# Performance work log

Hardware: AMD Instinct MI355X
Metric: run time of the kernel (lower is better)

## Reference

```python
import jax, jax.numpy as jnp
import numpy as np

B_SZ, L_SEQ, D_MODEL, D_STATE = 4, 2048, 1024, 16


def setup_inputs() -> dict:
    key = jax.random.key(0)
    ks = jax.random.split(key, 6)
    x = jax.random.normal(ks[0], (B_SZ, L_SEQ, D_MODEL), jnp.float32)
    # HiPPO-inspired init: A_log = log(arange(1..n)).clamp(min=-7), broadcast over channels
    A_log = jnp.clip(jnp.log(jnp.arange(1, D_STATE + 1, dtype=jnp.float32)), -7.0, None)
    A_log = jnp.broadcast_to(A_log[None, :], (D_MODEL, D_STATE)).astype(jnp.float32)
    B_param = 0.02 * jax.random.normal(ks[1], (D_MODEL, D_STATE), jnp.float32)
    C_param = 0.02 * jax.random.normal(ks[2], (D_MODEL, D_STATE), jnp.float32)
    log_dt = 0.01 * jax.random.normal(ks[3], (D_MODEL,), jnp.float32) - 4.0
    in_w = jax.random.normal(ks[4], (2 * D_MODEL, D_MODEL), jnp.float32) / np.sqrt(D_MODEL).astype(np.float32)
    in_b = jnp.zeros((2 * D_MODEL,), jnp.float32)
    out_w = jax.random.normal(ks[5], (D_MODEL, D_MODEL), jnp.float32) / np.sqrt(D_MODEL).astype(np.float32)
    out_b = jnp.zeros((D_MODEL,), jnp.float32)
    ln_g = jnp.ones((D_MODEL,), jnp.float32)
    ln_b = jnp.zeros((D_MODEL,), jnp.float32)
    return {"x": x, "A_log": A_log, "B_param": B_param, "C_param": C_param,
            "log_dt": log_dt, "in_w": in_w, "in_b": in_b, "out_w": out_w,
            "out_b": out_b, "ln_g": ln_g, "ln_b": ln_b}


def _ssm_scan(u, A_log, B_param, C_param, log_dt):
    # u: (B, L, D). Builds kernel h[t,d] = sum_n A_bar[d,n]^t * C[d,n]*B[d,n]*dt[d]
    # and applies a causal depthwise convolution (via FFT; same math as conv1d).
    L = u.shape[1]
    dt = jnp.clip(jnp.exp(log_dt), 1e-4, 1.0)                      # (D,)
    A_bar = jnp.exp(-jnp.exp(A_log) * dt[:, None])                 # ZOH discretisation (D,N)
    A_bar = jnp.clip(A_bar, 1e-8, 1.0 - 1e-8)
    log_A = jnp.log(A_bar)                                         # (D,N)
    t_idx = jnp.arange(L, dtype=jnp.float32)                       # (L,)
    A_powers = jnp.exp(t_idx[:, None, None] * log_A[None, :, :])   # (L,D,N)
    cb_dt = C_param * B_param * dt[:, None]                        # (D,N)
    kernel = jnp.einsum('ldn,dn->ld', A_powers, cb_dt)             # (L,D)
    # causal conv: y[b,t,d] = sum_{tau<=t} kernel[tau,d] * u[b,t-tau,d]
    n_fft = 2 * L
    Kf = jnp.fft.rfft(kernel, n=n_fft, axis=0)                     # (n_fft/2+1, D)
    Uf = jnp.fft.rfft(u, n=n_fft, axis=1)                          # (B, n_fft/2+1, D)
    y = jnp.fft.irfft(Uf * Kf[None], n=n_fft, axis=1)[:, :L]       # (B,L,D)
    return y.astype(u.dtype)


def reference(x, A_log, B_param, C_param, log_dt, in_w, in_b, out_w, out_b, ln_g, ln_b):
    x = x.astype(jnp.float32)
    residual = x
    # LayerNorm (eps=1e-5)
    mu = jnp.mean(x, axis=-1, keepdims=True)
    var = jnp.mean(jnp.square(x - mu), axis=-1, keepdims=True)
    xn = (x - mu) * jax.lax.rsqrt(var + 1e-5) * ln_g + ln_b
    xz = xn @ in_w.T + in_b                                        # (B,L,2D)
    x_proj, z = xz[..., :D_MODEL], xz[..., D_MODEL:]
    z = jax.nn.silu(z)
    y = _ssm_scan(x_proj, A_log, B_param, C_param, log_dt)
    y = y * z
    y = y @ out_w.T + out_b
    # dropout is identity in eval mode
    return jnp.clip(y + residual, -10.0, 10.0)
```

## Files before the change

kernel.cpp:

```cpp
#include <hip/hip_runtime.h>
#include <hip/hip_bf16.h>

#define D_MODEL 1024
#define D_STATE 16
#define L_SEQ 2048
#define B_SZ 4
#define M_ROWS (B_SZ * L_SEQ)
#define N_CHUNK 32
#define C_LEN 64

typedef __attribute__((ext_vector_type(8))) short short8;
typedef __attribute__((ext_vector_type(4))) float f32x4;

#define SBAR()  asm volatile("s_barrier" ::: "memory")
#define GATE(N) asm volatile("s_waitcnt vmcnt(" #N ") lgkmcnt(0)\n\ts_barrier" ::: "memory")

typedef const unsigned short __attribute__((address_space(1))) gas_us;
typedef unsigned short __attribute__((address_space(3))) las_us;
static __device__ __forceinline__ void gload16(const unsigned short* g, unsigned short* l) {
    __builtin_amdgcn_global_load_lds((gas_us*)g, (las_us*)l, 16, 0, 0);
}

static __device__ __forceinline__ unsigned short f2bf(float f) {
    unsigned int u = __float_as_uint(f);
    unsigned int r = (u + 0x7FFFu + ((u >> 16) & 1u)) >> 16;
    return (unsigned short)r;
}
static __device__ __forceinline__ float bf2f(unsigned short u) {
    return __uint_as_float(((unsigned int)u) << 16);
}

__global__ __launch_bounds__(256) void prep_kernel(const float* __restrict__ x,
                                                   const float* __restrict__ g,
                                                   const float* __restrict__ b,
                                                   unsigned short* __restrict__ xn,
                                                   const float* __restrict__ in_w,
                                                   unsigned short* __restrict__ w1,
                                                   const float* __restrict__ out_w,
                                                   unsigned short* __restrict__ w2) {
    __shared__ float sbuf[8];
    int bid = blockIdx.x;
    int t = threadIdx.x;
    if (bid < M_ROWS) {
        int row = bid;
        const float4* xr = (const float4*)(x + (size_t)row * D_MODEL);
        float4 v = xr[t];
        float s  = v.x + v.y + v.z + v.w;
        float ss = v.x * v.x + v.y * v.y + v.z * v.z + v.w * v.w;
        #pragma unroll
        for (int o = 32; o > 0; o >>= 1) {
            s  += __shfl_down(s,  o);
            ss += __shfl_down(ss, o);
        }
        int wid = t >> 6;
        if ((t & 63) == 0) { sbuf[wid] = s; sbuf[4 + wid] = ss; }
        __syncthreads();
        float S  = sbuf[0] + sbuf[1] + sbuf[2] + sbuf[3];
        float SS = sbuf[4] + sbuf[5] + sbuf[6] + sbuf[7];
        float mu  = S * (1.0f / D_MODEL);
        float var = SS * (1.0f / D_MODEL) - mu * mu;
        float inv = rsqrtf(var + 1e-5f);
        float4 gv = ((const float4*)g)[t];
        float4 bv = ((const float4*)b)[t];
        ushort4 o;
        o.x = f2bf((v.x - mu) * inv * gv.x + bv.x);
        o.y = f2bf((v.y - mu) * inv * gv.y + bv.y);
        o.z = f2bf((v.z - mu) * inv * gv.z + bv.z);
        o.w = f2bf((v.w - mu) * inv * gv.w + bv.w);
        ((ushort4*)(xn + (size_t)row * D_MODEL))[t] = o;
    } else if (bid < M_ROWS + 2048) {
        int i = (bid - M_ROWS) * 256 + t;
        float4 v = ((const float4*)in_w)[i];
        ushort4 o;
        o.x = f2bf(v.x); o.y = f2bf(v.y); o.z = f2bf(v.z); o.w = f2bf(v.w);
        ((ushort4*)w1)[i] = o;
    } else {
        int i = (bid - M_ROWS - 2048) * 256 + t;
        float4 v = ((const float4*)out_w)[i];
        ushort4 o;
        o.x = f2bf(v.x); o.y = f2bf(v.y); o.z = f2bf(v.z); o.w = f2bf(v.w);
        ((ushort4*)w2)[i] = o;
    }
}

#define MFMA32(ACC, AV, BV) { \
    _Pragma("unroll") for (int i_ = 0; i_ < 8; ++i_) { \
        _Pragma("unroll") for (int jf_ = 0; jf_ < 4; ++jf_) \
            ACC[i_][jf_] = __builtin_amdgcn_mfma_f32_16x16x32_bf16( \
                AV[i_], BV[jf_], ACC[i_][jf_], 0, 0, 0); } }

#define STAGE1(J) { size_t ko_ = (size_t)(J) * 32; int so_ = ((J) & 3) * 16384; \
    gload16(pA0 + ko_, dA0 + so_); gload16(pA1 + ko_, dA1 + so_); \
    gload16(pB0 + ko_, dB0 + so_); gload16(pB1 + ko_, dB1 + so_); }

#define G1_TILE(J, DOSTAGE, TRAIL) { \
    const int slot_ = (J) & 3; \
    const char* rA_ = ldsA_rd + slot_ * 32768; \
    const char* rB_ = ldsB_rd + slot_ * 32768; \
    short8 av[8], bv[4]; \
    _Pragma("unroll") for (int i_ = 0; i_ < 8; ++i_) av[i_] = *(const short8*)(rA_ + i_ * 1024); \
    _Pragma("unroll") for (int j_ = 0; j_ < 4; ++j_) bv[j_] = *(const short8*)(rB_ + j_ * 1024); \
    if (DOSTAGE) { STAGE1((J) + 3); } \
    SBAR(); \
    __builtin_amdgcn_s_setprio(1); \
    MFMA32(acc, av, bv); \
    __builtin_amdgcn_s_setprio(0); \
    TRAIL; \
}

__global__ __launch_bounds__(512, 1) void gemm1_kernel(const unsigned short* __restrict__ A,
                                                       const unsigned short* __restrict__ Bt,
                                                       const float* __restrict__ bias,
                                                       unsigned short* __restrict__ u_bf,
                                                       unsigned short* __restrict__ zs) {
    __shared__ __align__(16) unsigned short lds[4][16384];
    const int K = D_MODEL;

    int t = threadIdx.x;
    int lane = t & 63;
    int wave = t >> 6;
    int wm = wave >> 2;
    int wn = wave & 3;

    int bid = blockIdx.x;
    int swz = (bid & 7) * 32 + (bid >> 3);
    int m0 = (swz >> 3) * 256;
    int n0 = (swz & 7) * 256;

    int srow = lane >> 2;
    int sk = ((lane & 3) * 8) ^ ((lane & 32) >> 1);
    const unsigned short* pA0 = A  + (size_t)(m0 + wave * 16 + srow) * K + sk;
    const unsigned short* pA1 = pA0 + (size_t)128 * K;
    const unsigned short* pB0 = Bt + (size_t)(n0 + wave * 16 + srow) * K + sk;
    const unsigned short* pB1 = pB0 + (size_t)128 * K;

    unsigned short* dA0 = &lds[0][wave * 512];
    unsigned short* dA1 = &lds[0][4096 + wave * 512];
    unsigned short* dB0 = &lds[0][8192 + wave * 512];
    unsigned short* dB1 = &lds[0][12288 + wave * 512];

    int off_base = (lane & 15) * 64 + (((lane >> 4) * 16) ^ ((lane & 8) * 4));
    const char* ldsA_rd = (const char*)(&lds[0][0]) + wm * 8192 + off_base;
    const char* ldsB_rd = (const char*)(&lds[0][0]) + 16384 + wn * 4096 + off_base;

    f32x4 acc[8][4] = {};

    STAGE1(0); STAGE1(1); STAGE1(2);
    GATE(8);

    #pragma unroll 1
    for (int j = 0; j < 29; ++j) { G1_TILE(j, true, GATE(8)); }
    G1_TILE(29, false, GATE(4));
    G1_TILE(30, false, GATE(0));
    G1_TILE(31, false, (void)0);

    int col = lane & 15;
    int quad = lane >> 4;
    float bs[4];
    #pragma unroll
    for (int jf = 0; jf < 4; ++jf) bs[jf] = bias[n0 + wn * 64 + jf * 16 + col];
    bool isU = (n0 < D_MODEL);
    int nbase = isU ? (n0 + wn * 64 + col) : (n0 - D_MODEL + wn * 64 + col);
    unsigned short* obase = isU ? u_bf : zs;
    #pragma unroll
    for (int i = 0; i < 8; ++i) {
        #pragma unroll
        for (int r = 0; r < 4; ++r) {
            int m = m0 + wm * 128 + i * 16 + quad * 4 + r;
            unsigned short* orow = obase + (size_t)m * D_MODEL + nbase;
            #pragma unroll
            for (int jf = 0; jf < 4; ++jf) {
                float v = acc[i][jf][r] + bs[jf];
                if (!isU) v = v / (1.0f + __expf(-v));
                orow[jf * 16] = f2bf(v);
            }
        }
    }
}

#define MFMA16(ACC, AV, BV) { \
    _Pragma("unroll") for (int i_ = 0; i_ < 4; ++i_) { \
        _Pragma("unroll") for (int jf_ = 0; jf_ < 4; ++jf_) \
            ACC[i_][jf_] = __builtin_amdgcn_mfma_f32_16x16x32_bf16( \
                AV[i_], BV[jf_], ACC[i_][jf_], 0, 0, 0); } }

#define STAGE2(J) { size_t ko_ = (size_t)(J) * 32; int so_ = ((J) & 3) * 12288; \
    gload16(pA0 + ko_, dA + so_); gload16(pB0 + ko_, dB0 + so_); gload16(pB1 + ko_, dB1 + so_); }

#define G2_TILE(J, DOSTAGE, TRAIL) { \
    const int slot_ = (J) & 3; \
    const char* rA_ = ldsA_rd + slot_ * 24576; \
    const char* rB_ = ldsB_rd + slot_ * 24576; \
    short8 av[4], bv[4]; \
    _Pragma("unroll") for (int i_ = 0; i_ < 4; ++i_) av[i_] = *(const short8*)(rA_ + i_ * 1024); \
    _Pragma("unroll") for (int j_ = 0; j_ < 4; ++j_) bv[j_] = *(const short8*)(rB_ + j_ * 1024); \
    if (DOSTAGE) { STAGE2((J) + 3); } \
    SBAR(); \
    __builtin_amdgcn_s_setprio(1); \
    MFMA16(acc, av, bv); \
    __builtin_amdgcn_s_setprio(0); \
    TRAIL; \
}

__global__ __launch_bounds__(512, 2) void gemm2_kernel(const unsigned short* __restrict__ A,
                                                       const unsigned short* __restrict__ Bt,
                                                       const float* __restrict__ bias,
                                                       float* __restrict__ out_f,
                                                       const float* __restrict__ resid) {
    __shared__ __align__(16) unsigned short lds[4][12288];
    const int K = D_MODEL;

    int t = threadIdx.x;
    int lane = t & 63;
    int wave = t >> 6;
    int wm = wave >> 2;
    int wn = wave & 3;

    int bid = blockIdx.x;
    int swz = (bid & 7) * 32 + (bid >> 3);
    int m0 = (swz >> 2) * 128;
    int n0 = (swz & 3) * 256;

    int srow = lane >> 2;
    int sk = ((lane & 3) * 8) ^ ((lane & 32) >> 1);
    const unsigned short* pA0 = A  + (size_t)(m0 + wave * 16 + srow) * K + sk;
    const unsigned short* pB0 = Bt + (size_t)(n0 + wave * 16 + srow) * K + sk;
    const unsigned short* pB1 = pB0 + (size_t)128 * K;

    unsigned short* dA  = &lds[0][wave * 512];
    unsigned short* dB0 = &lds[0][4096 + wave * 512];
    unsigned short* dB1 = &lds[0][8192 + wave * 512];

    int off_base = (lane & 15) * 64 + (((lane >> 4) * 16) ^ ((lane & 8) * 4));
    const char* ldsA_rd = (const char*)(&lds[0][0]) + wm * 4096 + off_base;
    const char* ldsB_rd = (const char*)(&lds[0][0]) + 8192 + wn * 4096 + off_base;

    f32x4 acc[4][4] = {};

    STAGE2(0); STAGE2(1); STAGE2(2);
    GATE(6);

    #pragma unroll 1
    for (int j = 0; j < 29; ++j) { G2_TILE(j, true, GATE(6)); }
    G2_TILE(29, false, GATE(3));
    G2_TILE(30, false, GATE(0));
    G2_TILE(31, false, (void)0);

    int col = lane & 15;
    int quad = lane >> 4;
    float bs[4];
    #pragma unroll
    for (int jf = 0; jf < 4; ++jf) bs[jf] = bias[n0 + wn * 64 + jf * 16 + col];
    #pragma unroll
    for (int i = 0; i < 4; ++i) {
        #pragma unroll
        for (int r = 0; r < 4; ++r) {
            int m = m0 + wm * 64 + i * 16 + quad * 4 + r;
            const float* rrow = resid + (size_t)m * D_MODEL + n0 + wn * 64 + col;
            float* orow = out_f + (size_t)m * D_MODEL + n0 + wn * 64 + col;
            #pragma unroll
            for (int jf = 0; jf < 4; ++jf) {
                float y = acc[i][jf][r] + bs[jf] + rrow[jf * 16];
                y = fminf(10.0f, fmaxf(-10.0f, y));
                orow[jf * 16] = y;
            }
        }
    }
}

__global__ __launch_bounds__(512) void scan_fused_kernel(const unsigned short* __restrict__ u,
                                                         const unsigned short* __restrict__ zs,
                                                         const float* __restrict__ A_log,
                                                         const float* __restrict__ Bp,
                                                         const float* __restrict__ Cp,
                                                         const float* __restrict__ log_dt,
                                                         unsigned short* __restrict__ yz) {
    __shared__ float S[N_CHUNK][D_STATE][17];

    int bid = blockIdx.x;
    int l  = (bid & 7) * 32 + (bid >> 3);
    int b  = l >> 6;
    int dg = l & 63;
    int t  = threadIdx.x;
    int c  = t >> 4;
    int dl = t & 15;
    int d  = dg * 16 + dl;

    float dt = fminf(1.0f, fmaxf(1e-4f, __expf(log_dt[d])));
    float ab[D_STATE];
    #pragma unroll
    for (int n = 0; n < D_STATE; n++) {
        float a = __expf(-__expf(A_log[d * D_STATE + n]) * dt);
        ab[n] = fminf(1.0f - 1e-8f, fmaxf(1e-8f, a));
    }

    size_t row0 = (size_t)(b * L_SEQ + c * C_LEN);
    const unsigned short* up = u + row0 * D_MODEL + d;

    unsigned int uc[32];
    float P[D_STATE];
    #pragma unroll
    for (int n = 0; n < D_STATE; n++) P[n] = 0.0f;
    #pragma unroll
    for (int tt = 0; tt < 32; tt++) {
        unsigned int lo = up[(size_t)(2 * tt) * D_MODEL];
        unsigned int hi = up[(size_t)(2 * tt + 1) * D_MODEL];
        uc[tt] = lo | (hi << 16);
        float u0 = __uint_as_float(lo << 16);
        float u1 = __uint_as_float(hi << 16);
        #pragma unroll
        for (int n = 0; n < D_STATE; n++) P[n] = fmaf(ab[n], P[n], u0);
        #pragma unroll
        for (int n = 0; n < D_STATE; n++) P[n] = fmaf(ab[n], P[n], u1);
    }

    #pragma unroll
    for (int n = 0; n < D_STATE; n++) S[c][n][dl] = P[n];

    float m[D_STATE];
    #pragma unroll
    for (int n = 0; n < D_STATE; n++) {
        float a2 = ab[n];
        #pragma unroll
        for (int q = 0; q < 6; q++) a2 = a2 * a2;
        m[n] = a2;
    }
    __syncthreads();

    #pragma unroll
    for (int k = 1; k < N_CHUNK; k <<= 1) {
        float tmp[D_STATE];
        #pragma unroll
        for (int n = 0; n < D_STATE; n++) tmp[n] = (c >= k) ? S[c - k][n][dl] : 0.0f;
        __syncthreads();
        #pragma unroll
        for (int n = 0; n < D_STATE; n++) {
            P[n] = fmaf(m[n], tmp[n], P[n]);
            S[c][n][dl] = P[n];
        }
        #pragma unroll
        for (int n = 0; n < D_STATE; n++) m[n] = m[n] * m[n];
        __syncthreads();
    }

    float s2[D_STATE];
    #pragma unroll
    for (int n = 0; n < D_STATE; n++) s2[n] = (c == 0) ? 0.0f : S[c - 1][n][dl];

    float cb[D_STATE];
    #pragma unroll
    for (int n = 0; n < D_STATE; n++)
        cb[n] = Cp[d * D_STATE + n] * Bp[d * D_STATE + n] * dt;

    const unsigned short* zp = zs + row0 * D_MODEL + d;
    unsigned short* yp = yz + row0 * D_MODEL + d;

    #pragma unroll
    for (int tt = 0; tt < 32; tt++) {
        unsigned int w = uc[tt];
        float u0 = __uint_as_float(w << 16);
        float u1 = __uint_as_float(w & 0xFFFF0000u);
        float y0 = 0.0f, y1 = 0.0f;
        #pragma unroll
        for (int n = 0; n < D_STATE; n++) s2[n] = fmaf(ab[n], s2[n], u0);
        #pragma unroll
        for (int n = 0; n < D_STATE; n++) y0 = fmaf(cb[n], s2[n], y0);
        #pragma unroll
        for (int n = 0; n < D_STATE; n++) s2[n] = fmaf(ab[n], s2[n], u1);
        #pragma unroll
        for (int n = 0; n < D_STATE; n++) y1 = fmaf(cb[n], s2[n], y1);
        float z0 = bf2f(zp[(size_t)(2 * tt) * D_MODEL]);
        float z1 = bf2f(zp[(size_t)(2 * tt + 1) * D_MODEL]);
        yp[(size_t)(2 * tt) * D_MODEL]     = f2bf(y0 * z0);
        yp[(size_t)(2 * tt + 1) * D_MODEL] = f2bf(y1 * z1);
    }
}

extern "C" void kernel_launch(void* const* d_in, const int* in_sizes, int n_in,
                              void* d_out, int out_size, void* d_ws, size_t ws_size,
                              hipStream_t stream) {
    const float* x       = (const float*)d_in[0];
    const float* A_log   = (const float*)d_in[1];
    const float* B_param = (const float*)d_in[2];
    const float* C_param = (const float*)d_in[3];
    const float* log_dt  = (const float*)d_in[4];
    const float* in_w    = (const float*)d_in[5];
    const float* in_b    = (const float*)d_in[6];
    const float* out_w   = (const float*)d_in[7];
    const float* out_b   = (const float*)d_in[8];
    const float* ln_g    = (const float*)d_in[9];
    const float* ln_b    = (const float*)d_in[10];
    float* out = (float*)d_out;

    char* ws = (char*)d_ws;
    size_t off = 0;
    unsigned short* xn = (unsigned short*)(ws + off); off += (size_t)M_ROWS * D_MODEL * 2;
    unsigned short* w1 = (unsigned short*)(ws + off); off += (size_t)2 * D_MODEL * D_MODEL * 2;
    unsigned short* u  = (unsigned short*)(ws + off); off += (size_t)M_ROWS * D_MODEL * 2;
    unsigned short* zs = (unsigned short*)(ws + off); off += (size_t)M_ROWS * D_MODEL * 2;
    unsigned short* yz = (unsigned short*)(ws + off); off += (size_t)M_ROWS * D_MODEL * 2;
    unsigned short* w2 = (unsigned short*)(ws + off); off += (size_t)D_MODEL * D_MODEL * 2;

    prep_kernel<<<M_ROWS + 2048 + 1024, 256, 0, stream>>>(x, ln_g, ln_b, xn, in_w, w1, out_w, w2);

    gemm1_kernel<<<256, 512, 0, stream>>>(xn, w1, in_b, u, zs);

    scan_fused_kernel<<<256, 512, 0, stream>>>(u, zs, A_log, B_param, C_param, log_dt, yz);

    gemm2_kernel<<<256, 512, 0, stream>>>(yz, w2, out_b, out, x);
}
```

Before: 198.1 us.

## Shrink gemm1 tile to 128x256 with 3-stage LDS ring and more blocks

Reduces the first GEMM's output tile from 256x256 to 128x256 and doubles the grid to 512 blocks. The LDS pipeline goes from 4 slots to a 3-slot rotating ring, and launch bounds now allow multiple blocks per CU. The aim is to fill all CUs on MI355X (256 blocks left it near one wave) and hide latency through occupancy. In exchange, each block loads a larger share of B per output element, so arithmetic intensity drops, and the shallower prefetch depth leaves less latency hidden within a block.

```diff
diff --git a/kernel.cpp b/kernel.cpp
--- a/kernel.cpp
+++ b/kernel.cpp
@@ -83,37 +83,18 @@
     }
 }
 
-#define MFMA32(ACC, AV, BV) { \
-    _Pragma("unroll") for (int i_ = 0; i_ < 8; ++i_) { \
+#define MFMA16(ACC, AV, BV) { \
+    _Pragma("unroll") for (int i_ = 0; i_ < 4; ++i_) { \
         _Pragma("unroll") for (int jf_ = 0; jf_ < 4; ++jf_) \
             ACC[i_][jf_] = __builtin_amdgcn_mfma_f32_16x16x32_bf16( \
                 AV[i_], BV[jf_], ACC[i_][jf_], 0, 0, 0); } }
 
-#define STAGE1(J) { size_t ko_ = (size_t)(J) * 32; int so_ = ((J) & 3) * 16384; \
-    gload16(pA0 + ko_, dA0 + so_); gload16(pA1 + ko_, dA1 + so_); \
-    gload16(pB0 + ko_, dB0 + so_); gload16(pB1 + ko_, dB1 + so_); }
-
-#define G1_TILE(J, DOSTAGE, TRAIL) { \
-    const int slot_ = (J) & 3; \
-    const char* rA_ = ldsA_rd + slot_ * 32768; \
-    const char* rB_ = ldsB_rd + slot_ * 32768; \
-    short8 av[8], bv[4]; \
-    _Pragma("unroll") for (int i_ = 0; i_ < 8; ++i_) av[i_] = *(const short8*)(rA_ + i_ * 1024); \
-    _Pragma("unroll") for (int j_ = 0; j_ < 4; ++j_) bv[j_] = *(const short8*)(rB_ + j_ * 1024); \
-    if (DOSTAGE) { STAGE1((J) + 3); } \
-    SBAR(); \
-    __builtin_amdgcn_s_setprio(1); \
-    MFMA32(acc, av, bv); \
-    __builtin_amdgcn_s_setprio(0); \
-    TRAIL; \
-}
-
-__global__ __launch_bounds__(512, 1) void gemm1_kernel(const unsigned short* __restrict__ A,
+__global__ __launch_bounds__(512, 4) void gemm1_kernel(const unsigned short* __restrict__ A,
                                                        const unsigned short* __restrict__ Bt,
                                                        const float* __restrict__ bias,
                                                        unsigned short* __restrict__ u_bf,
                                                        unsigned short* __restrict__ zs) {
-    __shared__ __align__(16) unsigned short lds[4][16384];
+    __shared__ __align__(16) unsigned short lds[3][12288];
     const int K = D_MODEL;
 
     int t = threadIdx.x;
@@ -123,36 +104,82 @@
     int wn = wave & 3;
 
     int bid = blockIdx.x;
-    int swz = (bid & 7) * 32 + (bid >> 3);
-    int m0 = (swz >> 3) * 256;
+    int swz = (bid & 7) * 64 + (bid >> 3);
+    int m0 = (swz >> 3) * 128;
     int n0 = (swz & 7) * 256;
 
     int srow = lane >> 2;
     int sk = ((lane & 3) * 8) ^ ((lane & 32) >> 1);
     const unsigned short* pA0 = A  + (size_t)(m0 + wave * 16 + srow) * K + sk;
-    const unsigned short* pA1 = pA0 + (size_t)128 * K;
     const unsigned short* pB0 = Bt + (size_t)(n0 + wave * 16 + srow) * K + sk;
     const unsigned short* pB1 = pB0 + (size_t)128 * K;
 
-    unsigned short* dA0 = &lds[0][wave * 512];
-    unsigned short* dA1 = &lds[0][4096 + wave * 512];
-    unsigned short* dB0 = &lds[0][8192 + wave * 512];
-    unsigned short* dB1 = &lds[0][12288 + wave * 512];
+    unsigned short* dA  = &lds[0][0] + wave * 512;
+    unsigned short* dB0 = &lds[0][0] + 4096 + wave * 512;
+    unsigned short* dB1 = &lds[0][0] + 8192 + wave * 512;
 
     int off_base = (lane & 15) * 64 + (((lane >> 4) * 16) ^ ((lane & 8) * 4));
-    const char* ldsA_rd = (const char*)(&lds[0][0]) + wm * 8192 + off_base;
-    const char* ldsB_rd = (const char*)(&lds[0][0]) + 16384 + wn * 4096 + off_base;
-
-    f32x4 acc[8][4] = {};
-
-    STAGE1(0); STAGE1(1); STAGE1(2);
-    GATE(8);
-
+    const char* ldsA_rd = (const char*)(&lds[0][0]) + wm * 4096 + off_base;
+    const char* ldsB_rd = (const char*)(&lds[0][0]) + 8192 + wn * 4096 + off_base;
+
+    f32x4 acc[4][4] = {};
+
+    gload16(pA0, dA);      gload16(pB0, dB0);          gload16(pB1, dB1);
+    gload16(pA0 + 32, dA + 12288); gload16(pB0 + 32, dB0 + 12288); gload16(pB1 + 32, dB1 + 12288);
+    GATE(3);
+
+    int rs = 0, ws = 2;
+    size_t ko = 64;
     #pragma unroll 1
-    for (int j = 0; j < 29; ++j) { G1_TILE(j, true, GATE(8)); }
-    G1_TILE(29, false, GATE(4));
-    G1_TILE(30, false, GATE(0));
-    G1_TILE(31, false, (void)0);
+    for (int j = 0; j < 30; ++j) {
+        const char* rA_ = ldsA_rd + rs * 24576;
+        const char* rB_ = ldsB_rd + rs * 24576;
+        short8 av[4], bv[4];
+        #pragma unroll
+        for (int i_ = 0; i_ < 4; ++i_) av[i_] = *(const short8*)(rA_ + i_ * 1024);
+        #pragma unroll
+        for (int j_ = 0; j_ < 4; ++j_) bv[j_] = *(const short8*)(rB_ + j_ * 1024);
+        int wso = ws * 12288;
+        gload16(pA0 + ko, dA + wso);
+        gload16(pB0 + ko, dB0 + wso);
+        gload16(pB1 + ko, dB1 + wso);
+        SBAR();
+        __builtin_amdgcn_s_setprio(1);
+        MFMA16(acc, av, bv);
+        __builtin_amdgcn_s_setprio(0);
+        GATE(3);
+        rs = (rs == 2) ? 0 : rs + 1;
+        ws = (ws == 2) ? 0 : ws + 1;
+        ko += 32;
+    }
+    {
+        const char* rA_ = ldsA_rd + rs * 24576;
+        const char* rB_ = ldsB_rd + rs * 24576;
+        short8 av[4], bv[4];
+        #pragma unroll
+        for (int i_ = 0; i_ < 4; ++i_) av[i_] = *(const short8*)(rA_ + i_ * 1024);
+        #pragma unroll
+        for (int j_ = 0; j_ < 4; ++j_) bv[j_] = *(const short8*)(rB_ + j_ * 1024);
+        SBAR();
+        __builtin_amdgcn_s_setprio(1);
+        MFMA16(acc, av, bv);
+        __builtin_amdgcn_s_setprio(0);
+        GATE(0);
+        rs = (rs == 2) ? 0 : rs + 1;
+    }
+    {
+        const char* rA_ = ldsA_rd + rs * 24576;
+        const char* rB_ = ldsB_rd + rs * 24576;
+        short8 av[4], bv[4];
+        #pragma unroll
+        for (int i_ = 0; i_ < 4; ++i_) av[i_] = *(const short8*)(rA_ + i_ * 1024);
+        #pragma unroll
+        for (int j_ = 0; j_ < 4; ++j_) bv[j_] = *(const short8*)(rB_ + j_ * 1024);
+        SBAR();
+        __builtin_amdgcn_s_setprio(1);
+        MFMA16(acc, av, bv);
+        __builtin_amdgcn_s_setprio(0);
+    }
 
     int col = lane & 15;
     int quad = lane >> 4;
@@ -163,10 +190,10 @@
     int nbase = isU ? (n0 + wn * 64 + col) : (n0 - D_MODEL + wn * 64 + col);
     unsigned short* obase = isU ? u_bf : zs;
     #pragma unroll
-    for (int i = 0; i < 8; ++i) {
+    for (int i = 0; i < 4; ++i) {
         #pragma unroll
         for (int r = 0; r < 4; ++r) {
-            int m = m0 + wm * 128 + i * 16 + quad * 4 + r;
+            int m = m0 + wm * 64 + i * 16 + quad * 4 + r;
             unsigned short* orow = obase + (size_t)m * D_MODEL + nbase;
             #pragma unroll
             for (int jf = 0; jf < 4; ++jf) {
@@ -177,12 +204,6 @@
         }
     }
 }
-
-#define MFMA16(ACC, AV, BV) { \
-    _Pragma("unroll") for (int i_ = 0; i_ < 4; ++i_) { \
-        _Pragma("unroll") for (int jf_ = 0; jf_ < 4; ++jf_) \
-            ACC[i_][jf_] = __builtin_amdgcn_mfma_f32_16x16x32_bf16( \
-                AV[i_], BV[jf_], ACC[i_][jf_], 0, 0, 0); } }
 
 #define STAGE2(J) { size_t ko_ = (size_t)(J) * 32; int so_ = ((J) & 3) * 12288; \
     gload16(pA0 + ko_, dA + so_); gload16(pB0 + ko_, dB0 + so_); gload16(pB1 + ko_, dB1 + so_); }
@@ -403,7 +424,7 @@
 
     prep_kernel<<<M_ROWS + 2048 + 1024, 256, 0, stream>>>(x, ln_g, ln_b, xn, in_w, w1, out_w, w2);
 
-    gemm1_kernel<<<256, 512, 0, stream>>>(xn, w1, in_b, u, zs);
+    gemm1_kernel<<<512, 512, 0, stream>>>(xn, w1, in_b, u, zs);
 
     scan_fused_kernel<<<256, 512, 0, stream>>>(u, zs, A_log, B_param, C_param, log_dt, yz);
 
```

Result: faster. 193.8 us (-2.2%).

## Restructure gemm1 main loop into half-tile phases with double-buffered 64-K LDS stages

Applied to the files above, without the earlier changes.

Replaces the four-slot, 32-K-per-step LDS ring in the input-projection GEMM with two 64-K buffers, each split into A/B and two K-halves. Each iteration is issued as eight phases that each compute half of the M fragments. Global-to-LDS loads are interleaved per phase, one A or B half per phase, and barriers are placed between phases. The goal is finer-grained overlap of LDS reads, async global loads and MFMA work with smaller register live ranges. In exchange it adds more barriers and explicit lgkmcnt waits per K step.

```diff
diff --git a/kernel.cpp b/kernel.cpp
--- a/kernel.cpp
+++ b/kernel.cpp
@@ -83,29 +83,29 @@
     }
 }
 
-#define MFMA32(ACC, AV, BV) { \
-    _Pragma("unroll") for (int i_ = 0; i_ < 8; ++i_) { \
-        _Pragma("unroll") for (int jf_ = 0; jf_ < 4; ++jf_) \
-            ACC[i_][jf_] = __builtin_amdgcn_mfma_f32_16x16x32_bf16( \
-                AV[i_], BV[jf_], ACC[i_][jf_], 0, 0, 0); } }
-
-#define STAGE1(J) { size_t ko_ = (size_t)(J) * 32; int so_ = ((J) & 3) * 16384; \
-    gload16(pA0 + ko_, dA0 + so_); gload16(pA1 + ko_, dA1 + so_); \
-    gload16(pB0 + ko_, dB0 + so_); gload16(pB1 + ko_, dB1 + so_); }
-
-#define G1_TILE(J, DOSTAGE, TRAIL) { \
-    const int slot_ = (J) & 3; \
-    const char* rA_ = ldsA_rd + slot_ * 32768; \
-    const char* rB_ = ldsB_rd + slot_ * 32768; \
-    short8 av[8], bv[4]; \
-    _Pragma("unroll") for (int i_ = 0; i_ < 8; ++i_) av[i_] = *(const short8*)(rA_ + i_ * 1024); \
-    _Pragma("unroll") for (int j_ = 0; j_ < 4; ++j_) bv[j_] = *(const short8*)(rB_ + j_ * 1024); \
-    if (DOSTAGE) { STAGE1((J) + 3); } \
+#define STG(B_, MAT_, KH_, GPTR_, KOFF_) do { \
+    unsigned short* d_ = lbase + (B_)*32768 + (MAT_)*16384 + (KH_)*8192 + wave*1024; \
+    gload16((GPTR_) + (KOFF_), d_); \
+    gload16((GPTR_) + 16*K + (KOFF_), d_ + 512); } while(0)
+
+#define PH(B_, KS_, MG_, READB_, STAGE_, TAIL_) { \
+    if (READB_) { \
+        _Pragma("unroll") for (int j_ = 0; j_ < 4; ++j_) \
+            bv[j_] = *(const short8*)(ldsB + (B_)*65536 + (KS_)*16384 + (wn*4 + j_)*1024); \
+    } \
+    short8 av[4]; \
+    _Pragma("unroll") for (int i_ = 0; i_ < 4; ++i_) \
+        av[i_] = *(const short8*)(ldsA + (B_)*65536 + (KS_)*16384 + (wm*8 + (MG_)*4 + i_)*1024); \
+    STAGE_; \
     SBAR(); \
+    asm volatile("s_waitcnt lgkmcnt(0)" ::: "memory"); \
     __builtin_amdgcn_s_setprio(1); \
-    MFMA32(acc, av, bv); \
+    _Pragma("unroll") for (int i_ = 0; i_ < 4; ++i_) { \
+        _Pragma("unroll") for (int j_ = 0; j_ < 4; ++j_) \
+            acc[(MG_)*4 + i_][j_] = __builtin_amdgcn_mfma_f32_16x16x32_bf16( \
+                av[i_], bv[j_], acc[(MG_)*4 + i_][j_], 0, 0, 0); } \
     __builtin_amdgcn_s_setprio(0); \
-    TRAIL; \
+    TAIL_; \
 }
 
 __global__ __launch_bounds__(512, 1) void gemm1_kernel(const unsigned short* __restrict__ A,
@@ -113,7 +113,7 @@
                                                        const float* __restrict__ bias,
                                                        unsigned short* __restrict__ u_bf,
                                                        unsigned short* __restrict__ zs) {
-    __shared__ __align__(16) unsigned short lds[4][16384];
+    __shared__ __align__(16) unsigned short lds[2][32768];
     const int K = D_MODEL;
 
     int t = threadIdx.x;
@@ -129,30 +129,44 @@
 
     int srow = lane >> 2;
     int sk = ((lane & 3) * 8) ^ ((lane & 32) >> 1);
-    const unsigned short* pA0 = A  + (size_t)(m0 + wave * 16 + srow) * K + sk;
-    const unsigned short* pA1 = pA0 + (size_t)128 * K;
-    const unsigned short* pB0 = Bt + (size_t)(n0 + wave * 16 + srow) * K + sk;
-    const unsigned short* pB1 = pB0 + (size_t)128 * K;
-
-    unsigned short* dA0 = &lds[0][wave * 512];
-    unsigned short* dA1 = &lds[0][4096 + wave * 512];
-    unsigned short* dB0 = &lds[0][8192 + wave * 512];
-    unsigned short* dB1 = &lds[0][12288 + wave * 512];
+    const unsigned short* gA = A  + (size_t)(m0 + wave * 32 + srow) * K + sk;
+    const unsigned short* gB = Bt + (size_t)(n0 + wave * 32 + srow) * K + sk;
+
+    unsigned short* lbase = &lds[0][0];
 
     int off_base = (lane & 15) * 64 + (((lane >> 4) * 16) ^ ((lane & 8) * 4));
-    const char* ldsA_rd = (const char*)(&lds[0][0]) + wm * 8192 + off_base;
-    const char* ldsB_rd = (const char*)(&lds[0][0]) + 16384 + wn * 4096 + off_base;
+    const char* ldsA = (const char*)lbase + off_base;
+    const char* ldsB = (const char*)lbase + 32768 + off_base;
 
     f32x4 acc[8][4] = {};
-
-    STAGE1(0); STAGE1(1); STAGE1(2);
-    GATE(8);
-
+    short8 bv[4];
+
+    STG(0, 0, 0, gA, 0);  STG(0, 1, 0, gB, 0);
+    STG(0, 0, 1, gA, 32); STG(0, 1, 1, gB, 32);
+    STG(1, 0, 0, gA, 64); STG(1, 1, 0, gB, 64);
+    GATE(4);
+
+    int ko = 0;
     #pragma unroll 1
-    for (int j = 0; j < 29; ++j) { G1_TILE(j, true, GATE(8)); }
-    G1_TILE(29, false, GATE(4));
-    G1_TILE(30, false, GATE(0));
-    G1_TILE(31, false, (void)0);
+    for (int it = 0; it < 7; ++it) {
+        PH(0, 0, 0, true,  STG(1, 0, 1, gA, ko + 96),  SBAR());
+        PH(0, 0, 1, false, STG(1, 1, 1, gB, ko + 96),  SBAR());
+        PH(0, 1, 0, true,  STG(0, 0, 0, gA, ko + 128), SBAR());
+        PH(0, 1, 1, false, STG(0, 1, 0, gB, ko + 128), GATE(4));
+        PH(1, 0, 0, true,  STG(0, 0, 1, gA, ko + 160), SBAR());
+        PH(1, 0, 1, false, STG(0, 1, 1, gB, ko + 160), SBAR());
+        PH(1, 1, 0, true,  STG(1, 0, 0, gA, ko + 192), SBAR());
+        PH(1, 1, 1, false, STG(1, 1, 0, gB, ko + 192), GATE(4));
+        ko += 128;
+    }
+    PH(0, 0, 0, true,  STG(1, 0, 1, gA, ko + 96), SBAR());
+    PH(0, 0, 1, false, STG(1, 1, 1, gB, ko + 96), SBAR());
+    PH(0, 1, 0, true,  (void)0, SBAR());
+    PH(0, 1, 1, false, (void)0, GATE(0));
+    PH(1, 0, 0, true,  (void)0, SBAR());
+    PH(1, 0, 1, false, (void)0, SBAR());
+    PH(1, 1, 0, true,  (void)0, SBAR());
+    PH(1, 1, 1, false, (void)0, (void)0);
 
     int col = lane & 15;
     int quad = lane >> 4;
```

Measured after the change: 197.2 us (median of 2 runs). No clear change (-0.5%).
